# Performance work log

Measured on AMD Instinct MI355X. Metric: run time of the kernel, lower is better.

The kernel has to match this reference:

```python
import jax, jax.numpy as jnp
import numpy as np

B, H = 16384, 64          # batch, human_num
SELF_DIM, HUMAN_DIM = 6, 7
D = 32                    # gcn2_w1_dim / embedding dim


def _lin(key, fin, fout):
    return jax.random.normal(key, (fin, fout), jnp.float32) / np.sqrt(fin)


def setup_inputs() -> dict:
    key = jax.random.key(0)
    ks = jax.random.split(key, 40)
    inp = {}
    inp["state"] = jax.random.normal(ks[0], (B, H, SELF_DIM + HUMAN_DIM), jnp.float32)
    inp["dropout"] = 0
    # w_r: mlp(6 -> 64 -> 32, last_relu=True)
    inp["wr_w1"] = _lin(ks[1], SELF_DIM, 64); inp["wr_b1"] = jnp.zeros(64, jnp.float32)
    inp["wr_w2"] = _lin(ks[2], 64, D);        inp["wr_b2"] = jnp.zeros(D, jnp.float32)
    # w_h: mlp(7 -> 64 -> 32, last_relu=True)
    inp["wh_w1"] = _lin(ks[3], HUMAN_DIM, 64); inp["wh_b1"] = jnp.zeros(64, jnp.float32)
    inp["wh_w2"] = _lin(ks[4], 64, D);         inp["wh_b2"] = jnp.zeros(D, jnp.float32)
    # hetero GraphConv weights: per edge type (rh: robot->human, hr: human->robot, hh: human->human),
    # per layer. GraphConv: out = lin_rel(scatter_sum(x_src)) + lin_root(x_dst); lin_root has no bias.
    i = 5
    for L in (1, 2):
        for et in ("rh", "hr", "hh"):
            inp[f"rel_{et}{L}"] = _lin(ks[i], D, D); i += 1
            inp[f"brel_{et}{L}"] = jnp.zeros(D, jnp.float32)
            inp[f"root_{et}{L}"] = _lin(ks[i], D, D); i += 1
    # value_net: mlp(32 -> 150 -> 100 -> 1), no last relu
    inp["vn_w1"] = _lin(ks[i], D, 150);  inp["vn_b1"] = jnp.zeros(150, jnp.float32); i += 1
    inp["vn_w2"] = _lin(ks[i], 150, 100); inp["vn_b2"] = jnp.zeros(100, jnp.float32); i += 1
    inp["vn_w3"] = _lin(ks[i], 100, 1);  inp["vn_b3"] = jnp.zeros(1, jnp.float32)
    return inp


def _hetero_layer(r, h, rel_rh, brel_rh, root_rh, rel_hr, brel_hr, root_hr,
                  rel_hh, brel_hh, root_hh):
    # r: [B, D] robot nodes; h: [B, H, D] human nodes
    sum_h = h.sum(axis=1)  # [B, D]
    # robot receives scatter-sum over all humans (star graph, one robot target)
    new_r = jax.nn.relu(sum_h @ rel_hr + brel_hr + r @ root_hr)
    # each human receives: robot message + sum of all OTHER humans (full graph minus self-loops)
    agg_hh = sum_h[:, None, :] - h  # [B, H, D]
    new_h = jax.nn.relu((r @ rel_rh)[:, None, :] + brel_rh
                        + agg_hh @ rel_hh + brel_hh
                        + h @ root_rh + h @ root_hh)
    return new_r, new_h


def _forward(state, wr_w1, wr_b1, wr_w2, wr_b2, wh_w1, wh_b1, wh_w2, wh_b2,
             rel_rh1, brel_rh1, root_rh1, rel_hr1, brel_hr1, root_hr1,
             rel_hh1, brel_hh1, root_hh1,
             rel_rh2, brel_rh2, root_rh2, rel_hr2, brel_hr2, root_hr2,
             rel_hh2, brel_hh2, root_hh2,
             vn_w1, vn_b1, vn_w2, vn_b2, vn_w3, vn_b3):
    self_state = state[:, 0, :SELF_DIM]        # [B, 6]
    human_states = state[:, :, SELF_DIM:]      # [B, H, 7]
    r = jax.nn.relu(jax.nn.relu(self_state @ wr_w1 + wr_b1) @ wr_w2 + wr_b2)      # [B, D]
    h = jax.nn.relu(jax.nn.relu(human_states @ wh_w1 + wh_b1) @ wh_w2 + wh_b2)    # [B, H, D]
    r, h = _hetero_layer(r, h, rel_rh1, brel_rh1, root_rh1, rel_hr1, brel_hr1,
                         root_hr1, rel_hh1, brel_hh1, root_hh1)
    r, h = _hetero_layer(r, h, rel_rh2, brel_rh2, root_rh2, rel_hr2, brel_hr2,
                         root_hr2, rel_hh2, brel_hh2, root_hh2)
    v = jax.nn.relu(r @ vn_w1 + vn_b1)
    v = jax.nn.relu(v @ vn_w2 + vn_b2)
    return v @ vn_w3 + vn_b3                    # [B, 1]


def reference(state, dropout, wr_w1, wr_b1, wr_w2, wr_b2, wh_w1, wh_b1, wh_w2, wh_b2,
              rel_rh1, brel_rh1, root_rh1, rel_hr1, brel_hr1, root_hr1,
              rel_hh1, brel_hh1, root_hh1,
              rel_rh2, brel_rh2, root_rh2, rel_hr2, brel_hr2, root_hr2,
              rel_hh2, brel_hh2, root_hh2,
              vn_w1, vn_b1, vn_w2, vn_b2, vn_w3, vn_b3):
    # dropout is accepted but unused (matches the torch forward signature)
    return _forward(state, wr_w1, wr_b1, wr_w2, wr_b2, wh_w1, wh_b1, wh_w2, wh_b2,
                    rel_rh1, brel_rh1, root_rh1, rel_hr1, brel_hr1, root_hr1,
                    rel_hh1, brel_hh1, root_hh1,
                    rel_rh2, brel_rh2, root_rh2, rel_hr2, brel_hr2, root_hr2,
                    rel_hh2, brel_hh2, root_hh2,
                    vn_w1, vn_b1, vn_w2, vn_b2, vn_w3, vn_b3)
```

## Files before the change

kernel.cpp:

```cpp
#include <hip/hip_runtime.h>

#define BTOT 16384

typedef __attribute__((ext_vector_type(8))) short bf16x8;
typedef __attribute__((ext_vector_type(4))) float f32x4;

#define MFMA16(a,b,c) __builtin_amdgcn_mfma_f32_16x16x32_bf16((a),(b),(c),0,0,0)

static __device__ __forceinline__ short f2bf(float x) {
    unsigned u = __float_as_uint(x);
    unsigned r = (u + 0x7FFFu + ((u >> 16) & 1u)) >> 16;
    return (short)r;
}
static __device__ __forceinline__ bf16x8 zero8() {
    bf16x8 v;
    #pragma unroll
    for (int i = 0; i < 8; ++i) v[i] = 0;
    return v;
}

__global__ void pack_frags(const float* __restrict__ wh_w1, const float* __restrict__ wh_b1,
                           const float* __restrict__ wh_w2,
                           const float* __restrict__ root_rh1, const float* __restrict__ root_hh1,
                           const float* __restrict__ rel_hh1,
                           const float* __restrict__ vn_w1, const float* __restrict__ vn_w2,
                           short* __restrict__ pk) {
    int t = blockIdx.x * blockDim.x + threadIdx.x;
    if (t >= 28160) return;
    float val = 0.f;
    if (t < 2048) {
        int nt = t >> 9, r = t & 511, lane = r >> 3, j = r & 7;
        int q = lane >> 4, c = lane & 15;
        int k = q * 8 + j, n = nt * 16 + c;
        if (k < 7)       val = wh_w1[k * 64 + n];
        else if (k == 7) val = wh_b1[n];
    } else if (t < 4096) {
        int u = t - 2048;
        int kt = u >> 10; u &= 1023;
        int nt = u >> 9, r = u & 511, lane = r >> 3, j = r & 7;
        int q = lane >> 4, c = lane & 15;
        int k = kt * 32 + q * 8 + j, n = nt * 16 + c;
        val = wh_w2[k * 32 + n];
    } else if (t < 5120) {
        int u = t - 4096;
        int nt = u >> 9, r = u & 511, lane = r >> 3, j = r & 7;
        int q = lane >> 4, c = lane & 15;
        int k = q * 8 + j, n = nt * 16 + c;
        val = root_rh1[k * 32 + n] + root_hh1[k * 32 + n] - rel_hh1[k * 32 + n];
    } else if (t < 10240) {
        int u = t - 5120;
        int nt = u >> 9, r = u & 511, lane = r >> 3, j = r & 7;
        int q = lane >> 4, c = lane & 15;
        int k = q * 8 + j, n = nt * 16 + c;
        if (n < 150) val = vn_w1[k * 150 + n];
    } else {
        int u = t - 10240;
        int kt = u / 3584; u -= kt * 3584;
        int nt = u >> 9, r = u & 511, lane = r >> 3, j = r & 7;
        int q = lane >> 4, c = lane & 15;
        int k = kt * 32 + q * 8 + j, n = nt * 16 + c;
        if (k < 150 && n < 100) val = vn_w2[k * 100 + n];
    }
    pk[t] = f2bf(val);
}

__global__ __launch_bounds__(256) void fused_main(
    const float* __restrict__ state, const short* __restrict__ pk,
    const float* __restrict__ wr_w1, const float* __restrict__ wr_b1,
    const float* __restrict__ wr_w2, const float* __restrict__ wr_b2,
    const float* __restrict__ wh_b2,
    const float* __restrict__ rel_rh1, const float* __restrict__ brel_rh1,
    const float* __restrict__ rel_hr1, const float* __restrict__ brel_hr1,
    const float* __restrict__ root_hr1,
    const float* __restrict__ rel_hh1, const float* __restrict__ brel_hh1,
    const float* __restrict__ rel_hr2, const float* __restrict__ brel_hr2,
    const float* __restrict__ root_hr2,
    short* __restrict__ r2buf)
{
    __shared__ __align__(16) short sh_xa[4][64 * 8];
    __shared__ __align__(16) short sh_t [4][2 * 16 * 72];
    __shared__ __align__(16) short sh_h [4][64 * 40];
    __shared__ float sh_trh [4][64];
    __shared__ float sh_rr  [4][32];
    __shared__ float sh_sumh[4][32];
    __shared__ float sh_c1  [4][32];
    __shared__ float sh_r1  [4][32];
    __shared__ float sh_s2  [4][32];

    const int wv = threadIdx.x >> 6, lane = threadIdx.x & 63;
    const int q = lane >> 4, c = lane & 15;
    const int b = blockIdx.x * 4 + wv;
    const float* st = state + (size_t)b * 832;

    const bf16x8* wf = (const bf16x8*)pk;
    bf16x8 bw1[4], bw2[4], bwe[2];
    #pragma unroll
    for (int nt = 0; nt < 4; ++nt) bw1[nt] = wf[nt * 64 + lane];
    #pragma unroll
    for (int f = 0; f < 4; ++f)    bw2[f]  = wf[256 + f * 64 + lane];
    #pragma unroll
    for (int nt = 0; nt < 2; ++nt) bwe[nt] = wf[512 + nt * 64 + lane];

    short* xa = sh_xa[wv];
    #pragma unroll
    for (int i = 0; i < 13; ++i) {
        int idx = lane + 64 * i;
        float v = st[idx];
        int hu = idx / 13, f = idx - hu * 13;
        if (f >= 6) xa[hu * 8 + (f - 6)] = f2bf(v);
    }
    xa[lane * 8 + 7] = 0x3F80;

    {
        float acc = wr_b1[lane];
        #pragma unroll
        for (int m = 0; m < 6; ++m) acc = fmaf(st[m], wr_w1[m * 64 + lane], acc);
        sh_trh[wv][lane] = fmaxf(acc, 0.f);
    }
    __syncthreads();

    if (lane < 32) {
        float acc = wr_b2[lane];
        #pragma unroll
        for (int k = 0; k < 64; ++k) acc = fmaf(sh_trh[wv][k], wr_w2[k * 32 + lane], acc);
        sh_rr[wv][lane] = fmaxf(acc, 0.f);
    }

    const float b2a = wh_b2[c], b2b = wh_b2[16 + c];
    short* hb = sh_h[wv];
    const f32x4 z4 = {0.f, 0.f, 0.f, 0.f};
    float shp0 = 0.f, shp1 = 0.f;

    #pragma unroll
    for (int mt = 0; mt < 4; ++mt) {
        short* tb = sh_t[wv] + (mt & 1) * (16 * 72);
        bf16x8 a1 = zero8();
        if (q == 0) a1 = *(const bf16x8*)&xa[(mt * 16 + c) * 8];
        f32x4 d0 = MFMA16(a1, bw1[0], z4);
        f32x4 d1 = MFMA16(a1, bw1[1], z4);
        f32x4 d2 = MFMA16(a1, bw1[2], z4);
        f32x4 d3 = MFMA16(a1, bw1[3], z4);
        #pragma unroll
        for (int r = 0; r < 4; ++r) {
            tb[(q * 4 + r) * 72 +  0 + c] = f2bf(fmaxf(d0[r], 0.f));
            tb[(q * 4 + r) * 72 + 16 + c] = f2bf(fmaxf(d1[r], 0.f));
            tb[(q * 4 + r) * 72 + 32 + c] = f2bf(fmaxf(d2[r], 0.f));
            tb[(q * 4 + r) * 72 + 48 + c] = f2bf(fmaxf(d3[r], 0.f));
        }
        __syncthreads();
        bf16x8 a2k0 = *(const bf16x8*)&tb[c * 72 +  0 + q * 8];
        bf16x8 a2k1 = *(const bf16x8*)&tb[c * 72 + 32 + q * 8];
        f32x4 e0 = MFMA16(a2k0, bw2[0], z4); e0 = MFMA16(a2k1, bw2[2], e0);
        f32x4 e1 = MFMA16(a2k0, bw2[1], z4); e1 = MFMA16(a2k1, bw2[3], e1);
        #pragma unroll
        for (int r = 0; r < 4; ++r) {
            float v0 = fmaxf(e0[r] + b2a, 0.f), v1 = fmaxf(e1[r] + b2b, 0.f);
            hb[(mt * 16 + q * 4 + r) * 40 +  0 + c] = f2bf(v0);
            hb[(mt * 16 + q * 4 + r) * 40 + 16 + c] = f2bf(v1);
            shp0 += v0; shp1 += v1;
        }
    }
    shp0 += __shfl_xor(shp0, 16); shp0 += __shfl_xor(shp0, 32);
    shp1 += __shfl_xor(shp1, 16); shp1 += __shfl_xor(shp1, 32);
    if (lane < 16) { sh_sumh[wv][lane] = shp0; sh_sumh[wv][16 + lane] = shp1; }
    __syncthreads();

    if (lane < 32) {
        float a1 = 0.f, a2 = 0.f, ca = 0.f, cb = 0.f;
        #pragma unroll
        for (int k = 0; k < 32; ++k) {
            float sk = sh_sumh[wv][k], rk = sh_rr[wv][k];
            a1 = fmaf(sk, rel_hr1 [k * 32 + lane], a1);
            a2 = fmaf(rk, root_hr1[k * 32 + lane], a2);
            ca = fmaf(rk, rel_rh1 [k * 32 + lane], ca);
            cb = fmaf(sk, rel_hh1 [k * 32 + lane], cb);
        }
        sh_r1[wv][lane] = fmaxf(a1 + a2 + brel_hr1[lane], 0.f);
        sh_c1[wv][lane] = ca + cb + brel_rh1[lane] + brel_hh1[lane];
    }
    __syncthreads();

    const float c1a = sh_c1[wv][c], c1b = sh_c1[wv][16 + c];
    float s2p0 = 0.f, s2p1 = 0.f;
    #pragma unroll
    for (int mt = 0; mt < 4; ++mt) {
        bf16x8 a4 = *(const bf16x8*)&hb[(mt * 16 + c) * 40 + q * 8];
        f32x4 g0 = MFMA16(a4, bwe[0], z4);
        f32x4 g1 = MFMA16(a4, bwe[1], z4);
        #pragma unroll
        for (int r = 0; r < 4; ++r) {
            s2p0 += fmaxf(g0[r] + c1a, 0.f);
            s2p1 += fmaxf(g1[r] + c1b, 0.f);
        }
    }
    s2p0 += __shfl_xor(s2p0, 16); s2p0 += __shfl_xor(s2p0, 32);
    s2p1 += __shfl_xor(s2p1, 16); s2p1 += __shfl_xor(s2p1, 32);
    if (lane < 16) { sh_s2[wv][lane] = s2p0; sh_s2[wv][16 + lane] = s2p1; }
    __syncthreads();

    if (lane < 32) {
        float a1 = 0.f, a2 = 0.f;
        #pragma unroll
        for (int k = 0; k < 32; ++k) {
            a1 = fmaf(sh_s2[wv][k], rel_hr2 [k * 32 + lane], a1);
            a2 = fmaf(sh_r1[wv][k], root_hr2[k * 32 + lane], a2);
        }
        float r2 = fmaxf(a1 + a2 + brel_hr2[lane], 0.f);
        r2buf[b * 32 + lane] = f2bf(r2);
    }
}

__global__ __launch_bounds__(256) void head_kernel(
    const short* __restrict__ pk,
    const float* __restrict__ vn_b1, const float* __restrict__ vn_b2,
    const float* __restrict__ vn_w3, const float* __restrict__ vn_b3,
    float* __restrict__ out)
{
    __shared__ __align__(16) short sh_v1[4][16 * 168];
    const int wv = threadIdx.x >> 6, lane = threadIdx.x & 63;
    const int q = lane >> 4, c = lane & 15;
    const int tile = blockIdx.x * 4 + wv;
    const bf16x8* wf = (const bf16x8*)pk;
    const short* r2b = pk + 28672;
    const f32x4 z4 = {0.f, 0.f, 0.f, 0.f};

    bf16x8 a1 = *(const bf16x8*)&r2b[(tile * 16 + c) * 32 + q * 8];
    short* vb = sh_v1[wv];
    #pragma unroll
    for (int nt = 0; nt < 10; ++nt) {
        f32x4 d = MFMA16(a1, wf[640 + nt * 64 + lane], z4);
        int n = nt * 16 + c;
        float bias = (n < 150) ? vn_b1[n] : 0.f;
        #pragma unroll
        for (int r = 0; r < 4; ++r) {
            float v = (n < 150) ? fmaxf(d[r] + bias, 0.f) : 0.f;
            vb[(q * 4 + r) * 168 + n] = f2bf(v);
        }
    }
    __syncthreads();

    bf16x8 a2[5];
    #pragma unroll
    for (int kt = 0; kt < 5; ++kt)
        a2[kt] = *(const bf16x8*)&vb[c * 168 + kt * 32 + q * 8];

    float racc[4] = {0.f, 0.f, 0.f, 0.f};
    #pragma unroll
    for (int nt = 0; nt < 7; ++nt) {
        f32x4 d = z4;
        #pragma unroll
        for (int kt = 0; kt < 5; ++kt)
            d = MFMA16(a2[kt], wf[1280 + (kt * 7 + nt) * 64 + lane], d);
        int n = nt * 16 + c;
        float bias = (n < 100) ? vn_b2[n] : 0.f;
        float w3   = (n < 100) ? vn_w3[n] : 0.f;
        #pragma unroll
        for (int r = 0; r < 4; ++r) racc[r] += fmaxf(d[r] + bias, 0.f) * w3;
    }
    #pragma unroll
    for (int m = 1; m < 16; m <<= 1) {
        #pragma unroll
        for (int r = 0; r < 4; ++r) racc[r] += __shfl_xor(racc[r], m);
    }
    if (c == 0) {
        float b3 = vn_b3[0];
        #pragma unroll
        for (int r = 0; r < 4; ++r) out[tile * 16 + q * 4 + r] = racc[r] + b3;
    }
}

extern "C" void kernel_launch(void* const* d_in, const int* in_sizes, int n_in,
                              void* d_out, int out_size, void* d_ws, size_t ws_size,
                              hipStream_t stream) {
    const float* state    = (const float*)d_in[0];
    const float* wr_w1    = (const float*)d_in[2];
    const float* wr_b1    = (const float*)d_in[3];
    const float* wr_w2    = (const float*)d_in[4];
    const float* wr_b2    = (const float*)d_in[5];
    const float* wh_w1    = (const float*)d_in[6];
    const float* wh_b1    = (const float*)d_in[7];
    const float* wh_w2    = (const float*)d_in[8];
    const float* wh_b2    = (const float*)d_in[9];
    const float* rel_rh1  = (const float*)d_in[10];
    const float* brel_rh1 = (const float*)d_in[11];
    const float* root_rh1 = (const float*)d_in[12];
    const float* rel_hr1  = (const float*)d_in[13];
    const float* brel_hr1 = (const float*)d_in[14];
    const float* root_hr1 = (const float*)d_in[15];
    const float* rel_hh1  = (const float*)d_in[16];
    const float* brel_hh1 = (const float*)d_in[17];
    const float* root_hh1 = (const float*)d_in[18];
    const float* rel_hr2  = (const float*)d_in[22];
    const float* brel_hr2 = (const float*)d_in[23];
    const float* root_hr2 = (const float*)d_in[24];
    const float* vn_w1    = (const float*)d_in[28];
    const float* vn_b1    = (const float*)d_in[29];
    const float* vn_w2    = (const float*)d_in[30];
    const float* vn_b2    = (const float*)d_in[31];
    const float* vn_w3    = (const float*)d_in[32];
    const float* vn_b3    = (const float*)d_in[33];
    float* out = (float*)d_out;
    short* pk  = (short*)d_ws;
    short* r2buf = pk + 28672;

    pack_frags<<<110, 256, 0, stream>>>(wh_w1, wh_b1, wh_w2,
                                        root_rh1, root_hh1, rel_hh1,
                                        vn_w1, vn_w2, pk);
    fused_main<<<BTOT / 4, 256, 0, stream>>>(state, pk,
        wr_w1, wr_b1, wr_w2, wr_b2, wh_b2,
        rel_rh1, brel_rh1, rel_hr1, brel_hr1, root_hr1,
        rel_hh1, brel_hh1, rel_hr2, brel_hr2, root_hr2,
        r2buf);
    head_kernel<<<BTOT / 64, 256, 0, stream>>>(pk, vn_b1, vn_b2, vn_w3, vn_b3, out);
}
```

Baseline: 219.3 us.

## Move robot-path matvecs to MFMA with split-bf16 precision and consolidated LDS

Replaces the per-lane scalar fp32 matvec loops for wr_w2, the layer-1 robot/human-message transforms and the layer-2 robot update with MFMA tiles, batching the four batch elements of a block as rows. To keep accuracy, activations and weights are split into bf16 hi/lo pairs packed along K, so the products approximate fp32. The first human MLP layer is also transposed to remove a barrier per tile, and all shared buffers are merged into one per-wave region. This cuts scalar global weight loads and serial FMA chains, but makes wave 0 do the cross-wave work while the other waves idle at barriers.

```diff
diff --git a/kernel.cpp b/kernel.cpp
--- a/kernel.cpp
+++ b/kernel.cpp
@@ -7,10 +7,22 @@
 
 #define MFMA16(a,b,c) __builtin_amdgcn_mfma_f32_16x16x32_bf16((a),(b),(c),0,0,0)
 
-static __device__ __forceinline__ short f2bf(float x) {
+static __device__ __forceinline__ unsigned short bfhi(float x) {
     unsigned u = __float_as_uint(x);
-    unsigned r = (u + 0x7FFFu + ((u >> 16) & 1u)) >> 16;
-    return (short)r;
+    return (unsigned short)((u + 0x7FFFu + ((u >> 16) & 1u)) >> 16);
+}
+static __device__ __forceinline__ float b2f(unsigned short h) {
+    return __uint_as_float(((unsigned)h) << 16);
+}
+static __device__ __forceinline__ unsigned short bflo(float x) {
+    unsigned short h = bfhi(x);
+    return bfhi(x - b2f(h));
+}
+static __device__ __forceinline__ unsigned pk2(float a, float b) {
+    return (unsigned)bfhi(a) | ((unsigned)bfhi(b) << 16);
+}
+static __device__ __forceinline__ short f2s(float x) {
+    return (short)bfhi(x);
 }
 static __device__ __forceinline__ bf16x8 zero8() {
     bf16x8 v;
@@ -19,194 +31,301 @@
     return v;
 }
 
-__global__ void pack_frags(const float* __restrict__ wh_w1, const float* __restrict__ wh_b1,
-                           const float* __restrict__ wh_w2,
-                           const float* __restrict__ root_rh1, const float* __restrict__ root_hh1,
-                           const float* __restrict__ rel_hh1,
-                           const float* __restrict__ vn_w1, const float* __restrict__ vn_w2,
-                           short* __restrict__ pk) {
+__global__ void pack_frags(
+    const float* __restrict__ wh_w1, const float* __restrict__ wh_b1,
+    const float* __restrict__ wh_w2,
+    const float* __restrict__ root_rh1, const float* __restrict__ root_hh1,
+    const float* __restrict__ rel_hh1,
+    const float* __restrict__ wr_w2,
+    const float* __restrict__ rel_hr1, const float* __restrict__ root_hr1,
+    const float* __restrict__ rel_rh1,
+    const float* __restrict__ rel_hr2, const float* __restrict__ root_hr2,
+    const float* __restrict__ vn_w1, const float* __restrict__ vn_w2,
+    const float* __restrict__ brel_hr1, const float* __restrict__ brel_rh1,
+    const float* __restrict__ brel_hh1, const float* __restrict__ brel_hr2,
+    short* __restrict__ pk)
+{
     int t = blockIdx.x * blockDim.x + threadIdx.x;
-    if (t >= 28160) return;
-    float val = 0.f;
-    if (t < 2048) {
-        int nt = t >> 9, r = t & 511, lane = r >> 3, j = r & 7;
+    if (t < 52736) {
+        int f = t >> 9, r = t & 511;
+        int lane = r >> 3, j = r & 7;
         int q = lane >> 4, c = lane & 15;
-        int k = q * 8 + j, n = nt * 16 + c;
-        if (k < 7)       val = wh_w1[k * 64 + n];
-        else if (k == 7) val = wh_b1[n];
-    } else if (t < 4096) {
-        int u = t - 2048;
-        int kt = u >> 10; u &= 1023;
-        int nt = u >> 9, r = u & 511, lane = r >> 3, j = r & 7;
-        int q = lane >> 4, c = lane & 15;
-        int k = kt * 32 + q * 8 + j, n = nt * 16 + c;
-        val = wh_w2[k * 32 + n];
-    } else if (t < 5120) {
-        int u = t - 4096;
-        int nt = u >> 9, r = u & 511, lane = r >> 3, j = r & 7;
-        int q = lane >> 4, c = lane & 15;
-        int k = q * 8 + j, n = nt * 16 + c;
-        val = root_rh1[k * 32 + n] + root_hh1[k * 32 + n] - rel_hh1[k * 32 + n];
-    } else if (t < 10240) {
-        int u = t - 5120;
-        int nt = u >> 9, r = u & 511, lane = r >> 3, j = r & 7;
-        int q = lane >> 4, c = lane & 15;
-        int k = q * 8 + j, n = nt * 16 + c;
-        if (n < 150) val = vn_w1[k * 150 + n];
-    } else {
-        int u = t - 10240;
-        int kt = u / 3584; u -= kt * 3584;
-        int nt = u >> 9, r = u & 511, lane = r >> 3, j = r & 7;
-        int q = lane >> 4, c = lane & 15;
-        int k = kt * 32 + q * 8 + j, n = nt * 16 + c;
-        if (k < 150 && n < 100) val = vn_w2[k * 100 + n];
-    }
-    pk[t] = f2bf(val);
+        int k = q * 8 + j;
+        unsigned short outv;
+        if (f < 4) {
+            int m = f * 16 + c;
+            float v = (k < 7) ? wh_w1[k * 64 + m] : (k == 7 ? wh_b1[m] : 0.f);
+            outv = bfhi(v);
+        } else if (f < 8) {
+            int u = f - 4, ks = u >> 1, nt = u & 1;
+            outv = bfhi(wh_w2[(ks * 32 + k) * 32 + nt * 16 + c]);
+        } else if (f < 10) {
+            int n = (f - 8) * 16 + c;
+            outv = bfhi(root_rh1[k * 32 + n] + root_hh1[k * 32 + n] - rel_hh1[k * 32 + n]);
+        } else if (f < 22) {
+            int u = f - 10, ks = u >> 1, nt = u & 1;
+            int kp = ks * 32 + k;
+            float w = wr_w2[(kp & 63) * 32 + nt * 16 + c];
+            outv = (kp < 128) ? bfhi(w) : bflo(w);
+        } else if (f < 46) {
+            int u = f - 22, ks = u >> 2, nt = u & 3;
+            int kp = ks * 32 + k, seg = kp >> 5, kk = kp & 31;
+            int n2 = (nt & 1) * 16 + c;
+            bool sPart = (seg < 2) || (seg == 4);
+            const float* W = (nt < 2) ? (sPart ? rel_hr1 : root_hr1)
+                                      : (sPart ? rel_hh1 : rel_rh1);
+            float w = W[kk * 32 + n2];
+            outv = (seg < 4) ? bfhi(w) : bflo(w);
+        } else if (f < 58) {
+            int u = f - 46, ks = u >> 1, nt = u & 1;
+            int kp = ks * 32 + k, seg = kp >> 5, kk = kp & 31;
+            int n = nt * 16 + c;
+            bool sPart = (seg < 2) || (seg == 4);
+            const float* W = sPart ? rel_hr2 : root_hr2;
+            float w = W[kk * 32 + n];
+            outv = (seg < 4) ? bfhi(w) : bflo(w);
+        } else if (f < 68) {
+            int n = (f - 58) * 16 + c;
+            outv = (n < 150) ? bfhi(vn_w1[k * 150 + n]) : 0;
+        } else {
+            int u = f - 68, kt = u / 7, nt = u - kt * 7;
+            int kk = kt * 32 + k, n = nt * 16 + c;
+            outv = (kk < 150 && n < 100) ? bfhi(vn_w2[kk * 100 + n]) : 0;
+        }
+        pk[t] = (short)outv;
+    } else if (t < 52800) {
+        int i = t - 52736;
+        float* bp = (float*)(pk + 52736);
+        bp[i] = (i < 32) ? brel_hr1[i] : brel_rh1[i - 32] + brel_hh1[i - 32];
+    } else if (t < 52832) {
+        int i = t - 52800;
+        float* bp = (float*)(pk + 52864);
+        bp[i] = brel_hr2[i];
+    }
 }
 
 __global__ __launch_bounds__(256) void fused_main(
     const float* __restrict__ state, const short* __restrict__ pk,
     const float* __restrict__ wr_w1, const float* __restrict__ wr_b1,
-    const float* __restrict__ wr_w2, const float* __restrict__ wr_b2,
-    const float* __restrict__ wh_b2,
-    const float* __restrict__ rel_rh1, const float* __restrict__ brel_rh1,
-    const float* __restrict__ rel_hr1, const float* __restrict__ brel_hr1,
-    const float* __restrict__ root_hr1,
-    const float* __restrict__ rel_hh1, const float* __restrict__ brel_hh1,
-    const float* __restrict__ rel_hr2, const float* __restrict__ brel_hr2,
-    const float* __restrict__ root_hr2,
+    const float* __restrict__ wr_b2, const float* __restrict__ wh_b2,
     short* __restrict__ r2buf)
 {
-    __shared__ __align__(16) short sh_xa[4][64 * 8];
-    __shared__ __align__(16) short sh_t [4][2 * 16 * 72];
-    __shared__ __align__(16) short sh_h [4][64 * 40];
-    __shared__ float sh_trh [4][64];
-    __shared__ float sh_rr  [4][32];
-    __shared__ float sh_sumh[4][32];
-    __shared__ float sh_c1  [4][32];
-    __shared__ float sh_r1  [4][32];
-    __shared__ float sh_s2  [4][32];
-
-    const int wv = threadIdx.x >> 6, lane = threadIdx.x & 63;
+    __shared__ short wbuf[4][4608];
+
+    const int tid = threadIdx.x;
+    const int wv = tid >> 6, lane = tid & 63;
     const int q = lane >> 4, c = lane & 15;
     const int b = blockIdx.x * 4 + wv;
     const float* st = state + (size_t)b * 832;
-
-    const bf16x8* wf = (const bf16x8*)pk;
-    bf16x8 bw1[4], bw2[4], bwe[2];
-    #pragma unroll
-    for (int nt = 0; nt < 4; ++nt) bw1[nt] = wf[nt * 64 + lane];
-    #pragma unroll
-    for (int f = 0; f < 4; ++f)    bw2[f]  = wf[256 + f * 64 + lane];
-    #pragma unroll
-    for (int nt = 0; nt < 2; ++nt) bwe[nt] = wf[512 + nt * 64 + lane];
-
-    short* xa = sh_xa[wv];
-    #pragma unroll
-    for (int i = 0; i < 13; ++i) {
-        int idx = lane + 64 * i;
-        float v = st[idx];
-        int hu = idx / 13, f = idx - hu * 13;
-        if (f >= 6) xa[hu * 8 + (f - 6)] = f2bf(v);
-    }
-    xa[lane * 8 + 7] = 0x3F80;
-
+    short* T = wbuf[wv];
+
+    const bf16x8* pk16 = (const bf16x8*)pk;
+    const float* bg1f = (const float*)(pk + 52736);
+    const float* bg2f = (const float*)(pk + 52864);
+    const f32x4 z4 = {0.f, 0.f, 0.f, 0.f};
+
+    bf16x8 A1[4], Bh2v[4], Bev[2];
+    #pragma unroll
+    for (int i = 0; i < 4; ++i) A1[i] = pk16[i * 64 + lane];
+    #pragma unroll
+    for (int i = 0; i < 4; ++i) Bh2v[i] = pk16[(4 + i) * 64 + lane];
+    #pragma unroll
+    for (int i = 0; i < 2; ++i) Bev[i] = pk16[(8 + i) * 64 + lane];
+
+    {
+        float hf[7];
+        #pragma unroll
+        for (int m = 0; m < 7; ++m) hf[m] = st[lane * 13 + 6 + m];
+        uint4 v = make_uint4(pk2(hf[0], hf[1]), pk2(hf[2], hf[3]),
+                             pk2(hf[4], hf[5]), pk2(hf[6], 1.0f));
+        *(uint4*)(T + lane * 8) = v;
+    }
+
+    float trh;
     {
         float acc = wr_b1[lane];
         #pragma unroll
         for (int m = 0; m < 6; ++m) acc = fmaf(st[m], wr_w1[m * 64 + lane], acc);
-        sh_trh[wv][lane] = fmaxf(acc, 0.f);
-    }
-    __syncthreads();
-
-    if (lane < 32) {
-        float acc = wr_b2[lane];
-        #pragma unroll
-        for (int k = 0; k < 64; ++k) acc = fmaf(sh_trh[wv][k], wr_w2[k * 32 + lane], acc);
-        sh_rr[wv][lane] = fmaxf(acc, 0.f);
-    }
+        trh = fmaxf(acc, 0.f);
+    }
+
+    asm volatile("s_waitcnt lgkmcnt(0)" ::: "memory");
+
+    bf16x8 bx[4];
+    #pragma unroll
+    for (int ht = 0; ht < 4; ++ht) {
+        bf16x8 v = zero8();
+        if (q == 0) v = *(const bf16x8*)(T + (ht * 16 + c) * 8);
+        bx[ht] = v;
+    }
+
+    #pragma unroll
+    for (int mh = 0; mh < 4; ++mh) {
+        #pragma unroll
+        for (int ht = 0; ht < 4; ++ht) {
+            f32x4 d = MFMA16(A1[mh], bx[ht], z4);
+            uint2 w = make_uint2(pk2(fmaxf(d[0], 0.f), fmaxf(d[1], 0.f)),
+                                 pk2(fmaxf(d[2], 0.f), fmaxf(d[3], 0.f)));
+            *(uint2*)(T + (ht * 16 + c) * 72 + mh * 16 + q * 4) = w;
+        }
+    }
+
+    asm volatile("s_waitcnt lgkmcnt(0)" ::: "memory");
 
     const float b2a = wh_b2[c], b2b = wh_b2[16 + c];
-    short* hb = sh_h[wv];
-    const f32x4 z4 = {0.f, 0.f, 0.f, 0.f};
-    float shp0 = 0.f, shp1 = 0.f;
-
+    float ps0 = 0.f, ps1 = 0.f;
     #pragma unroll
     for (int mt = 0; mt < 4; ++mt) {
-        short* tb = sh_t[wv] + (mt & 1) * (16 * 72);
-        bf16x8 a1 = zero8();
-        if (q == 0) a1 = *(const bf16x8*)&xa[(mt * 16 + c) * 8];
-        f32x4 d0 = MFMA16(a1, bw1[0], z4);
-        f32x4 d1 = MFMA16(a1, bw1[1], z4);
-        f32x4 d2 = MFMA16(a1, bw1[2], z4);
-        f32x4 d3 = MFMA16(a1, bw1[3], z4);
-        #pragma unroll
-        for (int r = 0; r < 4; ++r) {
-            tb[(q * 4 + r) * 72 +  0 + c] = f2bf(fmaxf(d0[r], 0.f));
-            tb[(q * 4 + r) * 72 + 16 + c] = f2bf(fmaxf(d1[r], 0.f));
-            tb[(q * 4 + r) * 72 + 32 + c] = f2bf(fmaxf(d2[r], 0.f));
-            tb[(q * 4 + r) * 72 + 48 + c] = f2bf(fmaxf(d3[r], 0.f));
-        }
-        __syncthreads();
-        bf16x8 a2k0 = *(const bf16x8*)&tb[c * 72 +  0 + q * 8];
-        bf16x8 a2k1 = *(const bf16x8*)&tb[c * 72 + 32 + q * 8];
-        f32x4 e0 = MFMA16(a2k0, bw2[0], z4); e0 = MFMA16(a2k1, bw2[2], e0);
-        f32x4 e1 = MFMA16(a2k0, bw2[1], z4); e1 = MFMA16(a2k1, bw2[3], e1);
+        bf16x8 a0 = *(const bf16x8*)(T + (mt * 16 + c) * 72 + q * 8);
+        bf16x8 a1 = *(const bf16x8*)(T + (mt * 16 + c) * 72 + 32 + q * 8);
+        f32x4 e0 = MFMA16(a0, Bh2v[0], z4); e0 = MFMA16(a1, Bh2v[2], e0);
+        f32x4 e1 = MFMA16(a0, Bh2v[1], z4); e1 = MFMA16(a1, Bh2v[3], e1);
         #pragma unroll
         for (int r = 0; r < 4; ++r) {
             float v0 = fmaxf(e0[r] + b2a, 0.f), v1 = fmaxf(e1[r] + b2b, 0.f);
-            hb[(mt * 16 + q * 4 + r) * 40 +  0 + c] = f2bf(v0);
-            hb[(mt * 16 + q * 4 + r) * 40 + 16 + c] = f2bf(v1);
-            shp0 += v0; shp1 += v1;
-        }
-    }
-    shp0 += __shfl_xor(shp0, 16); shp0 += __shfl_xor(shp0, 32);
-    shp1 += __shfl_xor(shp1, 16); shp1 += __shfl_xor(shp1, 32);
-    if (lane < 16) { sh_sumh[wv][lane] = shp0; sh_sumh[wv][16 + lane] = shp1; }
+            int row = mt * 16 + q * 4 + r;
+            T[row * 40 + c]      = f2s(v0);
+            T[row * 40 + 16 + c] = f2s(v1);
+            ps0 += v0; ps1 += v1;
+        }
+    }
+    ps0 += __shfl_xor(ps0, 16); ps0 += __shfl_xor(ps0, 32);
+    ps1 += __shfl_xor(ps1, 16); ps1 += __shfl_xor(ps1, 32);
+
+    {
+        short* SB = T + 2816;
+        if (q == 0) {
+            unsigned short h0 = bfhi(ps0), h1 = bfhi(ps1);
+            SB[c] = (short)h0;        SB[16 + c] = (short)h1;
+            SB[32 + c] = (short)bfhi(ps0 - b2f(h0));
+            SB[48 + c] = (short)bfhi(ps1 - b2f(h1));
+            SB[128 + c] = (short)h0;  SB[144 + c] = (short)h1;
+        }
+        short* TR = T + 3008;
+        unsigned short th = bfhi(trh);
+        TR[lane] = (short)th;
+        TR[64 + lane] = (short)bfhi(trh - b2f(th));
+        TR[128 + lane] = (short)th;
+    }
     __syncthreads();
 
-    if (lane < 32) {
-        float a1 = 0.f, a2 = 0.f, ca = 0.f, cb = 0.f;
-        #pragma unroll
-        for (int k = 0; k < 32; ++k) {
-            float sk = sh_sumh[wv][k], rk = sh_rr[wv][k];
-            a1 = fmaf(sk, rel_hr1 [k * 32 + lane], a1);
-            a2 = fmaf(rk, root_hr1[k * 32 + lane], a2);
-            ca = fmaf(rk, rel_rh1 [k * 32 + lane], ca);
-            cb = fmaf(sk, rel_hh1 [k * 32 + lane], cb);
-        }
-        sh_r1[wv][lane] = fmaxf(a1 + a2 + brel_hr1[lane], 0.f);
-        sh_c1[wv][lane] = ca + cb + brel_rh1[lane] + brel_hh1[lane];
+    if (wv == 0) {
+        bf16x8 art[6];
+        #pragma unroll
+        for (int ks = 0; ks < 6; ++ks) {
+            bf16x8 v = zero8();
+            if (c < 4) v = *(const bf16x8*)(wbuf[c] + 3008 + ks * 32 + q * 8);
+            art[ks] = v;
+        }
+        f32x4 dr0 = z4, dr1 = z4;
+        #pragma unroll
+        for (int ks = 0; ks < 6; ++ks) {
+            dr0 = MFMA16(art[ks], pk16[(10 + ks * 2 + 0) * 64 + lane], dr0);
+            dr1 = MFMA16(art[ks], pk16[(10 + ks * 2 + 1) * 64 + lane], dr1);
+        }
+        const float wb0 = wr_b2[c], wb1 = wr_b2[16 + c];
+        if (q == 0) {
+            #pragma unroll
+            for (int r = 0; r < 4; ++r) {
+                float v0 = fmaxf(dr0[r] + wb0, 0.f), v1 = fmaxf(dr1[r] + wb1, 0.f);
+                short* SBr = wbuf[r] + 2816;
+                unsigned short h0 = bfhi(v0), h1 = bfhi(v1);
+                SBr[64 + c] = (short)h0;  SBr[96 + c]  = (short)bfhi(v0 - b2f(h0));  SBr[160 + c] = (short)h0;
+                SBr[80 + c] = (short)h1;  SBr[112 + c] = (short)bfhi(v1 - b2f(h1));  SBr[176 + c] = (short)h1;
+            }
+        }
+        asm volatile("s_waitcnt lgkmcnt(0)" ::: "memory");
+
+        bf16x8 ag[6];
+        #pragma unroll
+        for (int ks = 0; ks < 6; ++ks) {
+            bf16x8 v = zero8();
+            if (c < 4) v = *(const bf16x8*)(wbuf[c] + 2816 + ks * 32 + q * 8);
+            ag[ks] = v;
+        }
+        f32x4 dg[4] = {z4, z4, z4, z4};
+        #pragma unroll
+        for (int ks = 0; ks < 6; ++ks) {
+            #pragma unroll
+            for (int nt = 0; nt < 4; ++nt)
+                dg[nt] = MFMA16(ag[ks], pk16[(22 + ks * 4 + nt) * 64 + lane], dg[nt]);
+        }
+        if (q == 0) {
+            #pragma unroll
+            for (int nt = 0; nt < 2; ++nt) {
+                float bias = bg1f[nt * 16 + c];
+                #pragma unroll
+                for (int r = 0; r < 4; ++r) {
+                    float v = fmaxf(dg[nt][r] + bias, 0.f);
+                    short* G2r = wbuf[r] + 2624;
+                    unsigned short hh = bfhi(v);
+                    G2r[64 + nt * 16 + c]  = (short)hh;
+                    G2r[96 + nt * 16 + c]  = (short)bfhi(v - b2f(hh));
+                    G2r[160 + nt * 16 + c] = (short)hh;
+                }
+            }
+            #pragma unroll
+            for (int nt = 2; nt < 4; ++nt) {
+                float bias = bg1f[nt * 16 + c];
+                #pragma unroll
+                for (int r = 0; r < 4; ++r)
+                    ((float*)(wbuf[r] + 2560))[(nt - 2) * 16 + c] = dg[nt][r] + bias;
+            }
+        }
     }
     __syncthreads();
 
-    const float c1a = sh_c1[wv][c], c1b = sh_c1[wv][16 + c];
-    float s2p0 = 0.f, s2p1 = 0.f;
-    #pragma unroll
-    for (int mt = 0; mt < 4; ++mt) {
-        bf16x8 a4 = *(const bf16x8*)&hb[(mt * 16 + c) * 40 + q * 8];
-        f32x4 g0 = MFMA16(a4, bwe[0], z4);
-        f32x4 g1 = MFMA16(a4, bwe[1], z4);
-        #pragma unroll
-        for (int r = 0; r < 4; ++r) {
-            s2p0 += fmaxf(g0[r] + c1a, 0.f);
-            s2p1 += fmaxf(g1[r] + c1b, 0.f);
-        }
-    }
-    s2p0 += __shfl_xor(s2p0, 16); s2p0 += __shfl_xor(s2p0, 32);
-    s2p1 += __shfl_xor(s2p1, 16); s2p1 += __shfl_xor(s2p1, 32);
-    if (lane < 16) { sh_s2[wv][lane] = s2p0; sh_s2[wv][16 + lane] = s2p1; }
+    {
+        const float* C1 = (const float*)(T + 2560);
+        const float c10 = C1[c], c11 = C1[16 + c];
+        float t0 = 0.f, t1 = 0.f;
+        #pragma unroll
+        for (int mt = 0; mt < 4; ++mt) {
+            bf16x8 ah = *(const bf16x8*)(T + (mt * 16 + c) * 40 + q * 8);
+            f32x4 g0 = MFMA16(ah, Bev[0], z4);
+            f32x4 g1 = MFMA16(ah, Bev[1], z4);
+            #pragma unroll
+            for (int r = 0; r < 4; ++r) {
+                t0 += fmaxf(g0[r] + c10, 0.f);
+                t1 += fmaxf(g1[r] + c11, 0.f);
+            }
+        }
+        t0 += __shfl_xor(t0, 16); t0 += __shfl_xor(t0, 32);
+        t1 += __shfl_xor(t1, 16); t1 += __shfl_xor(t1, 32);
+        short* G2 = T + 2624;
+        if (q == 0) {
+            unsigned short h0 = bfhi(t0), h1 = bfhi(t1);
+            G2[c] = (short)h0;        G2[16 + c] = (short)h1;
+            G2[32 + c] = (short)bfhi(t0 - b2f(h0));
+            G2[48 + c] = (short)bfhi(t1 - b2f(h1));
+            G2[128 + c] = (short)h0;  G2[144 + c] = (short)h1;
+        }
+    }
     __syncthreads();
 
-    if (lane < 32) {
-        float a1 = 0.f, a2 = 0.f;
-        #pragma unroll
-        for (int k = 0; k < 32; ++k) {
-            a1 = fmaf(sh_s2[wv][k], rel_hr2 [k * 32 + lane], a1);
-            a2 = fmaf(sh_r1[wv][k], root_hr2[k * 32 + lane], a2);
-        }
-        float r2 = fmaxf(a1 + a2 + brel_hr2[lane], 0.f);
-        r2buf[b * 32 + lane] = f2bf(r2);
+    if (wv == 0) {
+        bf16x8 a2[6];
+        #pragma unroll
+        for (int ks = 0; ks < 6; ++ks) {
+            bf16x8 v = zero8();
+            if (c < 4) v = *(const bf16x8*)(wbuf[c] + 2624 + ks * 32 + q * 8);
+            a2[ks] = v;
+        }
+        f32x4 d0 = z4, d1 = z4;
+        #pragma unroll
+        for (int ks = 0; ks < 6; ++ks) {
+            d0 = MFMA16(a2[ks], pk16[(46 + ks * 2 + 0) * 64 + lane], d0);
+            d1 = MFMA16(a2[ks], pk16[(46 + ks * 2 + 1) * 64 + lane], d1);
+        }
+        if (q == 0) {
+            const int b0 = blockIdx.x * 4;
+            const float g0 = bg2f[c], g1 = bg2f[16 + c];
+            #pragma unroll
+            for (int r = 0; r < 4; ++r) {
+                r2buf[(b0 + r) * 32 + c]      = f2s(fmaxf(d0[r] + g0, 0.f));
+                r2buf[(b0 + r) * 32 + 16 + c] = f2s(fmaxf(d1[r] + g1, 0.f));
+            }
+        }
     }
 }
 
@@ -221,20 +340,20 @@
     const int q = lane >> 4, c = lane & 15;
     const int tile = blockIdx.x * 4 + wv;
     const bf16x8* wf = (const bf16x8*)pk;
-    const short* r2b = pk + 28672;
+    const short* r2b = pk + 53248;
     const f32x4 z4 = {0.f, 0.f, 0.f, 0.f};
 
     bf16x8 a1 = *(const bf16x8*)&r2b[(tile * 16 + c) * 32 + q * 8];
     short* vb = sh_v1[wv];
     #pragma unroll
     for (int nt = 0; nt < 10; ++nt) {
-        f32x4 d = MFMA16(a1, wf[640 + nt * 64 + lane], z4);
+        f32x4 d = MFMA16(a1, wf[(58 + nt) * 64 + lane], z4);
         int n = nt * 16 + c;
         float bias = (n < 150) ? vn_b1[n] : 0.f;
         #pragma unroll
         for (int r = 0; r < 4; ++r) {
             float v = (n < 150) ? fmaxf(d[r] + bias, 0.f) : 0.f;
-            vb[(q * 4 + r) * 168 + n] = f2bf(v);
+            vb[(q * 4 + r) * 168 + n] = f2s(v);
         }
     }
     __syncthreads();
@@ -250,7 +369,7 @@
         f32x4 d = z4;
         #pragma unroll
         for (int kt = 0; kt < 5; ++kt)
-            d = MFMA16(a2[kt], wf[1280 + (kt * 7 + nt) * 64 + lane], d);
+            d = MFMA16(a2[kt], wf[(68 + kt * 7 + nt) * 64 + lane], d);
         int n = nt * 16 + c;
         float bias = (n < 100) ? vn_b2[n] : 0.f;
         float w3   = (n < 100) ? vn_w3[n] : 0.f;
@@ -301,15 +420,13 @@
     const float* vn_b3    = (const float*)d_in[33];
     float* out = (float*)d_out;
     short* pk  = (short*)d_ws;
-    short* r2buf = pk + 28672;
-
-    pack_frags<<<110, 256, 0, stream>>>(wh_w1, wh_b1, wh_w2,
-                                        root_rh1, root_hh1, rel_hh1,
-                                        vn_w1, vn_w2, pk);
-    fused_main<<<BTOT / 4, 256, 0, stream>>>(state, pk,
-        wr_w1, wr_b1, wr_w2, wr_b2, wh_b2,
-        rel_rh1, brel_rh1, rel_hr1, brel_hr1, root_hr1,
-        rel_hh1, brel_hh1, rel_hr2, brel_hr2, root_hr2,
-        r2buf);
+    short* r2buf = pk + 53248;
+
+    pack_frags<<<207, 256, 0, stream>>>(wh_w1, wh_b1, wh_w2,
+                                        root_rh1, root_hh1, rel_hh1, wr_w2,
+                                        rel_hr1, root_hr1, rel_rh1,
+                                        rel_hr2, root_hr2, vn_w1, vn_w2,
+                                        brel_hr1, brel_rh1, brel_hh1, brel_hr2, pk);
+    fused_main<<<BTOT / 4, 256, 0, stream>>>(state, pk, wr_w1, wr_b1, wr_b2, wh_b2, r2buf);
     head_kernel<<<BTOT / 64, 256, 0, stream>>>(pk, vn_b1, vn_b2, vn_w3, vn_b3, out);
 }
```

After: 187.0 us. 14.7% less time.
